# Optimization experiments

Hardware: AMD Instinct MI355X
Metric: run time of the kernel (lower is better)

The kernel has to match this reference:

```python
import jax, jax.numpy as jnp
import numpy as np

B, T, C = 4, 4096, 512
H = 64           # head_size
GRAN = 128       # staircase granularity


def staircase_mask(t, g):
    # tril OR block-diagonal blocks of size g (the staircase fills the upper
    # triangle inside each gxg diagonal block)
    i = jnp.arange(t)
    return (i[:, None] >= i[None, :]) | ((i[:, None] // g) == (i[None, :] // g))


def setup_inputs() -> dict:
    key = jax.random.key(0)
    kx, kk, kq, kv = jax.random.split(key, 4)
    scale = 0.02
    return {
        "x": jax.random.normal(kx, (B, T, C), dtype=jnp.float32),
        "Wk": jax.random.normal(kk, (C, H), dtype=jnp.float32) * scale,
        "Wq": jax.random.normal(kq, (C, H), dtype=jnp.float32) * scale,
        "Wv": jax.random.normal(kv, (C, H), dtype=jnp.float32) * scale,
    }


def reference(x, Wk, Wq, Wv):
    # single head of self-attention with staircase mask (dropout off / eval mode)
    k = x @ Wk          # [B,T,H]
    q = x @ Wq          # [B,T,H]
    v = x @ Wv          # [B,T,H]
    wei = jnp.einsum("bth,bsh->bts", q, k) * (H ** -0.5)   # [B,T,T]
    mask = staircase_mask(T, GRAN)                           # [T,T] bool
    wei = jnp.where(mask, wei, -jnp.inf)
    wei = jax.nn.softmax(wei, axis=-1)
    out = jnp.einsum("bts,bsh->bth", wei, v)                 # [B,T,H]
    return out
```

## Files before the change

kernel.cpp:

```cpp
#include <hip/hip_runtime.h>

typedef unsigned short u16;
typedef unsigned int u32;
typedef unsigned long long u64;
typedef __attribute__((ext_vector_type(8))) short short8;
typedef __attribute__((ext_vector_type(4))) float f32x4;

#define T_ 4096
#define QSCALE 0.18033688f
#define CH 2
#define SBAT 1088
#define PSTRIDE 36

#if __has_builtin(__builtin_amdgcn_exp2f)
#define EXP2F(x) __builtin_amdgcn_exp2f(x)
#else
#define EXP2F(x) exp2f(x)
#endif

__device__ __forceinline__ u16 f2bf(float f) {
    unsigned u = __float_as_uint(f);
    u += 0x7FFFu + ((u >> 16) & 1u);
    return (u16)(u >> 16);
}

__global__ __launch_bounds__(256) void wtrans_kernel(
    const float* __restrict__ Wq, const float* __restrict__ Wk,
    const float* __restrict__ Wv, u16* __restrict__ WTf)
{
    const int tid  = blockIdx.x * 256 + threadIdx.x;
    const int frag = tid >> 6;
    const int lane = tid & 63;
    const int ng   = frag >> 4;
    const int kc   = frag & 15;
    const int m    = ng >> 2;
    const float* W = (m == 0) ? Wq : (m == 1) ? Wk : Wv;
    const int h  = (ng & 3) * 16 + (lane & 15);
    const int c0 = kc * 32 + (lane >> 4) * 8;
    short8 v;
    #pragma unroll
    for (int j = 0; j < 8; ++j)
        v[j] = (short)f2bf(W[(c0 + j) * 64 + h]);
    *(short8*)(WTf + (size_t)frag * 512 + lane * 8) = v;
}

__global__ __launch_bounds__(256) void proj_kernel(
    const float* __restrict__ x, const u16* __restrict__ WTf,
    u16* __restrict__ Qf, u16* __restrict__ Kf, u16* __restrict__ Vf)
{
    __shared__ u16 xs[16 * 520];
    __shared__ u16 img[3072];
    const int t    = threadIdx.x;
    const int lane = t & 63;
    const int w    = t >> 6;
    const int l16  = lane & 15;
    const int quad = lane >> 4;
    const int rowbase = blockIdx.x * 16;
    const int bat  = rowbase >> 12;
    const int tloc = rowbase & 4095;

    #pragma unroll
    for (int it = 0; it < 8; ++it) {
        int f   = t + it * 256;
        int row = f >> 7;
        int c4  = (f & 127) * 4;
        f32x4 a = *(const f32x4*)(x + (size_t)(rowbase + row) * 512 + c4);
        unsigned lo = (unsigned)f2bf(a[0]) | ((unsigned)f2bf(a[1]) << 16);
        unsigned hi = (unsigned)f2bf(a[2]) | ((unsigned)f2bf(a[3]) << 16);
        *(uint2*)(xs + row * 520 + c4) = make_uint2(lo, hi);
    }
    __syncthreads();

    f32x4 acc[3];
    #pragma unroll
    for (int nt = 0; nt < 3; ++nt) acc[nt] = (f32x4){0.f, 0.f, 0.f, 0.f};

    const u16* ab = xs + l16 * 520 + quad * 8;
    const u16* wb = WTf + (size_t)(w * 3 * 16) * 512 + lane * 8;

    #pragma unroll 4
    for (int kc = 0; kc < 16; ++kc) {
        short8 af = *(const short8*)(ab + kc * 32);
        #pragma unroll
        for (int nt = 0; nt < 3; ++nt) {
            short8 bf = *(const short8*)(wb + (size_t)(nt * 16 + kc) * 512);
            acc[nt] = __builtin_amdgcn_mfma_f32_16x16x32_bf16(af, bf, acc[nt], 0, 0, 0);
        }
    }

    #pragma unroll
    for (int nt = 0; nt < 3; ++nt) {
        int ng = w * 3 + nt;
        if (ng < 8) {
            int ng4  = ng & 3;
            float sc = (ng < 4) ? QSCALE : 1.0f;
            u16* ib  = img + ((ng < 4) ? 0 : 1024) + (ng4 >> 1) * 512
                          + ((ng4 & 1) * 2 + (l16 >> 3)) * 128 + (l16 & 7);
            #pragma unroll
            for (int i = 0; i < 4; ++i)
                ib[(quad * 4 + i) * 8] = f2bf(acc[nt][i] * sc);
        } else {
            int nt2  = ng - 8;
            unsigned lo = (unsigned)f2bf(acc[nt][0]) | ((unsigned)f2bf(acc[nt][1]) << 16);
            unsigned hi = (unsigned)f2bf(acc[nt][2]) | ((unsigned)f2bf(acc[nt][3]) << 16);
            *(uint2*)(img + 2048 + nt2 * 256 + (quad >> 1) * 128 + l16 * 8
                          + (quad & 1) * 4) = make_uint2(lo, hi);
        }
    }
    __syncthreads();

    const int tb   = tloc >> 4;
    const int kt   = tloc >> 7;
    const int ks   = (tloc >> 5) & 3;
    const int half = (tloc >> 4) & 1;
    uint2 vq = *(uint2*)(img + t * 4);
    uint2 vk = *(uint2*)(img + 1024 + t * 4);
    uint2 vv = *(uint2*)(img + 2048 + t * 4);
    *(uint2*)(Qf + (size_t)(bat * 256 + tb) * 1024 + t * 4) = vq;
    *(uint2*)(Kf + (size_t)(bat * 256 + tb) * 1024 + t * 4) = vk;
    const int nt2c = t >> 6;
    *(uint2*)(Vf + (size_t)((bat * 32 + kt) * 4 + ks) * 2048
                 + nt2c * 512 + half * 256 + (t & 63) * 4) = vv;
}

__global__ __launch_bounds__(256, 4) void attn_kernel(
    const u16* __restrict__ Qf, const u16* __restrict__ Kf,
    const u16* __restrict__ Vf, u32* __restrict__ pnum,
    float* __restrict__ pden, float* __restrict__ out)
{
    __shared__ u16 Ps[4][2][16 * PSTRIDE];

    const int w    = threadIdx.x >> 6;
    const int lane = threadIdx.x & 63;
    const int l16  = lane & 15;
    const int qd   = lane >> 4;
    const int xcd  = blockIdx.x & 7;
    const int bat  = xcd >> 1;
    const int tw   = ((blockIdx.x >> 3) * 2 + (xcd & 1)) * 4 + w;

    int A = 31, pre = 0, cc = 1;
    for (;;) {
        cc = (A + CH) / CH;
        int cnt4 = 4 * cc;
        if (tw < pre + cnt4) break;
        pre += cnt4; --A;
    }
    const int r    = tw - pre;
    const int c    = r >> 2;
    const int b_   = r & 3;
    const int nkt  = A + 1;
    const int q32  = 4 * A + b_;
    const int kt0  = c * CH;
    const int kt1  = min(kt0 + CH, nkt);
    const int slot = bat * SBAT + pre + b_ + 4 * c;

    short8 aq[2][2];
    #pragma unroll
    for (int g = 0; g < 2; ++g)
        #pragma unroll
        for (int f = 0; f < 2; ++f)
            aq[g][f] = *(const short8*)(Qf
                + ((size_t)((bat * 256 + q32 * 2 + g) * 2 + f)) * 512 + lane * 8);

    short8 ones;
    #pragma unroll
    for (int j = 0; j < 8; ++j) ones[j] = (short)0x3F80;

    f32x4 acc[2][4];
    f32x4 accden[2];
    #pragma unroll
    for (int g = 0; g < 2; ++g) {
        accden[g] = (f32x4){0.f, 0.f, 0.f, 0.f};
        for (int n = 0; n < 4; ++n) acc[g][n] = (f32x4){0.f, 0.f, 0.f, 0.f};
    }

    u16* Pw[2] = { &Ps[w][0][0], &Ps[w][1][0] };

    auto body = [&](int kt) __attribute__((always_inline)) {
        const u16* kfb = Kf + ((size_t)(bat * 256 + kt * 8) * 2) * 512 + lane * 8;
        const u16* vfb = Vf + ((size_t)((bat * 32 + kt) * 16)) * 512 + lane * 8;
        #pragma unroll
        for (int ks = 0; ks < 4; ++ks) {
            #pragma unroll
            for (int b = 0; b < 2; ++b) {
                int nt = 2 * ks + b;
                short8 k0 = *(const short8*)(kfb + (size_t)nt * 1024);
                short8 k1 = *(const short8*)(kfb + (size_t)nt * 1024 + 512);
                #pragma unroll
                for (int g = 0; g < 2; ++g) {
                    f32x4 st = (f32x4){0.f, 0.f, 0.f, 0.f};
                    st = __builtin_amdgcn_mfma_f32_16x16x32_bf16(k0, aq[g][0], st, 0, 0, 0);
                    st = __builtin_amdgcn_mfma_f32_16x16x32_bf16(k1, aq[g][1], st, 0, 0, 0);
                    float p0 = EXP2F(st[0]);
                    float p1 = EXP2F(st[1]);
                    float p2 = EXP2F(st[2]);
                    float p3 = EXP2F(st[3]);
                    u32 q01 = __builtin_amdgcn_perm(__float_as_uint(p1), __float_as_uint(p0), 0x07060302u);
                    u32 q23 = __builtin_amdgcn_perm(__float_as_uint(p3), __float_as_uint(p2), 0x07060302u);
                    u64 pv = (u64)q01 | ((u64)q23 << 32);
                    *(u64*)(Pw[g] + l16 * PSTRIDE + b * 16 + qd * 4) = pv;
                }
            }
            short8 ap[2];
            #pragma unroll
            for (int g = 0; g < 2; ++g)
                ap[g] = *(const short8*)(Pw[g] + l16 * PSTRIDE + qd * 8);
            accden[0] = __builtin_amdgcn_mfma_f32_16x16x32_bf16(ones, ap[0], accden[0], 0, 0, 0);
            accden[1] = __builtin_amdgcn_mfma_f32_16x16x32_bf16(ones, ap[1], accden[1], 0, 0, 0);
            #pragma unroll
            for (int nt2 = 0; nt2 < 4; ++nt2) {
                short8 av = *(const short8*)(vfb + (size_t)(ks * 4 + nt2) * 512);
                acc[0][nt2] = __builtin_amdgcn_mfma_f32_16x16x32_bf16(av, ap[0], acc[0][nt2], 0, 0, 0);
                acc[1][nt2] = __builtin_amdgcn_mfma_f32_16x16x32_bf16(av, ap[1], acc[1][nt2], 0, 0, 0);
            }
        }
    };

    body(kt0);
    if (kt0 + 1 < kt1) body(kt0 + 1);

    float den[2] = { accden[0][0], accden[1][0] };

    if (cc == 1) {
        const float rd0 = 1.0f / den[0];
        const float rd1 = 1.0f / den[1];
        float* op = out + ((size_t)(bat * T_ + q32 * 32 + l16)) * 64 + qd * 4;
        #pragma unroll
        for (int g = 0; g < 2; ++g) {
            const float rd = g ? rd1 : rd0;
            #pragma unroll
            for (int nt2 = 0; nt2 < 4; ++nt2) {
                f32x4 v;
                #pragma unroll
                for (int i = 0; i < 4; ++i) v[i] = acc[g][nt2][i] * rd;
                *(f32x4*)(op + (size_t)g * 16 * 64 + nt2 * 16) = v;
            }
        }
    } else {
        u32* np = pnum + (size_t)slot * 1024;
        #pragma unroll
        for (int g = 0; g < 2; ++g)
            #pragma unroll
            for (int nt2 = 0; nt2 < 4; ++nt2) {
                u32 lo = (u32)f2bf(acc[g][nt2][0]) | ((u32)f2bf(acc[g][nt2][1]) << 16);
                u32 hi = (u32)f2bf(acc[g][nt2][2]) | ((u32)f2bf(acc[g][nt2][3]) << 16);
                u64 val = (u64)lo | ((u64)hi << 32);
                __builtin_nontemporal_store(val, (u64*)(np + (g * 4 + nt2) * 128 + lane * 2));
            }
        if (lane < 32)
            __builtin_nontemporal_store(den[lane >> 4],
                                        &pden[(size_t)slot * 32 + lane]);
    }
}

__global__ __launch_bounds__(256) void fin_kernel(
    const u32* __restrict__ pnum, const float* __restrict__ pden,
    float* __restrict__ out)
{
    __shared__ float rden[32];
    const int bq  = blockIdx.x;
    const int bat = bq >> 7;
    const int q32 = bq & 127;
    const int A = q32 >> 2, b = q32 & 3;
    const int cc = (A + CH) / CH;
    if (cc == 1) return;
    int pre = 0;
    for (int j = 31; j > A; --j) pre += 4 * ((j + CH) / CH);
    const int base = bat * SBAT + pre + b;

    if (threadIdx.x < 32) {
        float d = 0.f;
        for (int ci = 0; ci < cc; ++ci)
            d += pden[(size_t)(base + 4 * ci) * 32 + threadIdx.x];
        rden[threadIdx.x] = 1.0f / d;
    }
    __syncthreads();

    const int m   = threadIdx.x >> 3;
    const int g   = m >> 4;
    const int l16 = m & 15;
    const int h0  = (threadIdx.x & 7) * 8;
    const int nt2 = h0 >> 4;
    const int q0  = (h0 >> 2) & 3;
    const int off = (g * 4 + nt2) * 128 + q0 * 32 + l16 * 2;

    float sv[8];
    #pragma unroll
    for (int e = 0; e < 8; ++e) sv[e] = 0.f;
    for (int ci = 0; ci < cc; ++ci) {
        const u32* sp = pnum + (size_t)(base + 4 * ci) * 1024 + off;
        uint2 a  = *(const uint2*)(sp);
        uint2 bb = *(const uint2*)(sp + 32);
        u32 vals[4] = {a.x, a.y, bb.x, bb.y};
        #pragma unroll
        for (int e = 0; e < 4; ++e) {
            sv[2 * e]     += __uint_as_float(vals[e] << 16);
            sv[2 * e + 1] += __uint_as_float(vals[e] & 0xFFFF0000u);
        }
    }
    const float rd = rden[m];
    float* op = out + (size_t)(bat * T_ + q32 * 32 + m) * 64 + h0;
    f32x4 r0, r1;
    #pragma unroll
    for (int i = 0; i < 4; ++i) { r0[i] = sv[i] * rd; r1[i] = sv[4 + i] * rd; }
    *(f32x4*)(op)     = r0;
    *(f32x4*)(op + 4) = r1;
}

extern "C" void kernel_launch(void* const* d_in, const int* in_sizes, int n_in,
                              void* d_out, int out_size, void* d_ws, size_t ws_size,
                              hipStream_t stream)
{
    const float* x  = (const float*)d_in[0];
    const float* Wk = (const float*)d_in[1];
    const float* Wq = (const float*)d_in[2];
    const float* Wv = (const float*)d_in[3];
    float* out = (float*)d_out;

    u16* ws  = (u16*)d_ws;
    u16* WTf = ws;
    u16* Qf  = ws + 131072;
    u16* Kf  = Qf + 1048576;
    u16* Vf  = Kf + 1048576;
    u32*   pnum = (u32*)(Vf + 1048576);
    float* pden = (float*)(pnum + (size_t)4 * SBAT * 1024);

    wtrans_kernel<<<48, 256, 0, stream>>>(Wq, Wk, Wv, WTf);
    proj_kernel<<<1024, 256, 0, stream>>>(x, WTf, Qf, Kf, Vf);
    attn_kernel<<<SBAT, 256, 0, stream>>>(Qf, Kf, Vf, pnum, pden, out);
    fin_kernel<<<512, 256, 0, stream>>>(pnum, pden, out);
}
```

Before: 122.3 us.

## Split finalize kernel across head halves with XCD-aware block mapping

```diff
diff --git a/kernel.cpp b/kernel.cpp
--- a/kernel.cpp
+++ b/kernel.cpp
@@ -257,10 +257,14 @@
     const u32* __restrict__ pnum, const float* __restrict__ pden,
     float* __restrict__ out)
 {
+    __shared__ float sden[8][32];
     __shared__ float rden[32];
-    const int bq  = blockIdx.x;
-    const int bat = bq >> 7;
-    const int q32 = bq & 127;
+    const int blk  = blockIdx.x;
+    const int xcd  = blk & 7;
+    const int bat  = xcd >> 1;
+    const int rest = blk >> 3;
+    const int q32  = (rest & 63) * 2 + (xcd & 1);
+    const int hh   = rest >> 6;
     const int A = q32 >> 2, b = q32 & 3;
     const int cc = (A + CH) / CH;
     if (cc == 1) return;
@@ -268,10 +272,19 @@
     for (int j = 31; j > A; --j) pre += 4 * ((j + CH) / CH);
     const int base = bat * SBAT + pre + b;
 
+    {
+        const int md  = threadIdx.x & 31;
+        const int grp = threadIdx.x >> 5;
+        float d = 0.f;
+        for (int ci = grp; ci < cc; ci += 8)
+            d += pden[(size_t)(base + 4 * ci) * 32 + md];
+        sden[grp][md] = d;
+    }
+    __syncthreads();
     if (threadIdx.x < 32) {
         float d = 0.f;
-        for (int ci = 0; ci < cc; ++ci)
-            d += pden[(size_t)(base + 4 * ci) * 32 + threadIdx.x];
+        #pragma unroll
+        for (int g2 = 0; g2 < 8; ++g2) d += sden[g2][threadIdx.x];
         rden[threadIdx.x] = 1.0f / d;
     }
     __syncthreads();
@@ -279,32 +292,32 @@
     const int m   = threadIdx.x >> 3;
     const int g   = m >> 4;
     const int l16 = m & 15;
-    const int h0  = (threadIdx.x & 7) * 8;
+    const int h0  = hh * 32 + (threadIdx.x & 7) * 4;
     const int nt2 = h0 >> 4;
     const int q0  = (h0 >> 2) & 3;
     const int off = (g * 4 + nt2) * 128 + q0 * 32 + l16 * 2;
 
-    float sv[8];
-    #pragma unroll
-    for (int e = 0; e < 8; ++e) sv[e] = 0.f;
-    for (int ci = 0; ci < cc; ++ci) {
-        const u32* sp = pnum + (size_t)(base + 4 * ci) * 1024 + off;
-        uint2 a  = *(const uint2*)(sp);
-        uint2 bb = *(const uint2*)(sp + 32);
-        u32 vals[4] = {a.x, a.y, bb.x, bb.y};
-        #pragma unroll
-        for (int e = 0; e < 4; ++e) {
-            sv[2 * e]     += __uint_as_float(vals[e] << 16);
-            sv[2 * e + 1] += __uint_as_float(vals[e] & 0xFFFF0000u);
-        }
-    }
+    float sv0 = 0.f, sv1 = 0.f, sv2 = 0.f, sv3 = 0.f;
+    const u32* sp = pnum + (size_t)base * 1024 + off;
+    uint2 cur = *(const uint2*)sp;
+    for (int ci = 1; ci < cc; ++ci) {
+        uint2 nxt = *(const uint2*)(sp + (size_t)ci * 4096);
+        sv0 += __uint_as_float(cur.x << 16);
+        sv1 += __uint_as_float(cur.x & 0xFFFF0000u);
+        sv2 += __uint_as_float(cur.y << 16);
+        sv3 += __uint_as_float(cur.y & 0xFFFF0000u);
+        cur = nxt;
+    }
+    sv0 += __uint_as_float(cur.x << 16);
+    sv1 += __uint_as_float(cur.x & 0xFFFF0000u);
+    sv2 += __uint_as_float(cur.y << 16);
+    sv3 += __uint_as_float(cur.y & 0xFFFF0000u);
+
     const float rd = rden[m];
     float* op = out + (size_t)(bat * T_ + q32 * 32 + m) * 64 + h0;
-    f32x4 r0, r1;
-    #pragma unroll
-    for (int i = 0; i < 4; ++i) { r0[i] = sv[i] * rd; r1[i] = sv[4 + i] * rd; }
-    *(f32x4*)(op)     = r0;
-    *(f32x4*)(op + 4) = r1;
+    f32x4 r;
+    r[0] = sv0 * rd; r[1] = sv1 * rd; r[2] = sv2 * rd; r[3] = sv3 * rd;
+    *(f32x4*)op = r;
 }
 
 extern "C" void kernel_launch(void* const* d_in, const int* in_sizes, int n_in,
@@ -328,5 +341,5 @@
     wtrans_kernel<<<48, 256, 0, stream>>>(Wq, Wk, Wv, WTf);
     proj_kernel<<<1024, 256, 0, stream>>>(x, WTf, Qf, Kf, Vf);
     attn_kernel<<<SBAT, 256, 0, stream>>>(Qf, Kf, Vf, pnum, pden, out);
-    fin_kernel<<<512, 256, 0, stream>>>(pnum, pden, out);
-}
+    fin_kernel<<<1024, 256, 0, stream>>>(pnum, pden, out);
+}
```

After: 118.0 us. -3.5%, faster.
